# Kernel tuning notes

Measured on AMD Instinct MI355X. Metric: run time of the kernel, lower is better.

Reference implementation:

```python
import jax, jax.numpy as jnp
import numpy as np

HIDDEN = 1024
NUM_EXPERTS = 8
TOP_K = 2
B, S = 4, 2048


def setup_inputs() -> dict:
    key = jax.random.key(0)
    ks = jax.random.split(key, 7)
    s = 0.02
    return {
        "x": jax.random.normal(ks[0], (B, S, HIDDEN), dtype=jnp.float32),
        "gate_w": jax.random.normal(ks[1], (NUM_EXPERTS, HIDDEN), dtype=jnp.float32) * s,
        "gate_b": jnp.zeros((NUM_EXPERTS,), dtype=jnp.float32),
        "w1": jax.random.normal(ks[2], (NUM_EXPERTS, 4 * HIDDEN, HIDDEN), dtype=jnp.float32) * s,
        "b1": jnp.zeros((NUM_EXPERTS, 4 * HIDDEN), dtype=jnp.float32),
        "w2": jax.random.normal(ks[3], (NUM_EXPERTS, HIDDEN, 4 * HIDDEN), dtype=jnp.float32) * s,
        "b2": jnp.zeros((NUM_EXPERTS, HIDDEN), dtype=jnp.float32),
    }


def reference(x, gate_w, gate_b, w1, b1, w2, b2):
    bsz, seq_len, hidden = x.shape
    T = bsz * seq_len
    flat = x.reshape(T, hidden)  # [T, H]

    gate_logits = flat @ gate_w.T + gate_b  # [T, E]
    topk_vals, topk_idx = jax.lax.top_k(gate_logits, TOP_K)  # [T, K]
    topk_w = jax.nn.softmax(topk_vals, axis=-1)  # [T, K]

    # combine[t, e] = routing weight of expert e for token t (0 if not selected)
    combine = jnp.zeros((T, NUM_EXPERTS), dtype=flat.dtype)
    combine = combine.at[jnp.arange(T)[:, None], topk_idx].add(topk_w)

    out_flat = jnp.zeros_like(flat)
    for e in range(NUM_EXPERTS):  # small fixed expert count
        h = jax.nn.gelu(flat @ w1[e].T + b1[e], approximate=False)  # [T, 4H]
        y = h @ w2[e].T + b2[e]  # [T, H]
        out_flat = out_flat + y * combine[:, e:e + 1]

    out = out_flat.reshape(bsz, seq_len, hidden)
    probs = jax.nn.softmax(gate_logits, axis=-1).mean(axis=0)  # [E]
    l_aux = (probs * probs).sum() * NUM_EXPERTS
    return out, l_aux
```

## Files before the change

### kernel.cpp

```cpp
#include <hip/hip_runtime.h>
#include <cstdint>
#include <cstddef>

typedef unsigned short u16;
typedef short bf16x8 __attribute__((ext_vector_type(8)));
typedef float f32x4 __attribute__((ext_vector_type(4)));
typedef u16 u16x4 __attribute__((ext_vector_type(4)));

#define NTOK 8192
#define HID 1024
#define NEXP 8
#define FF 4096
#define MAXPAIR 18432

__device__ __forceinline__ u16 bf16_rne(float f) {
  unsigned u = __builtin_bit_cast(unsigned, f);
  return (u16)((u + 0x7FFFu + ((u >> 16) & 1u)) >> 16);
}

__device__ __forceinline__ float gelu_tanh(float v) {
  const float u = 0.7978845608028654f * (v + 0.044715f * v * v * v);
  const float e = __expf(2.0f * u);
  return v - v * __frcp_rn(e + 1.0f);
}

__device__ __forceinline__ void async16(const void* g, void* l) {
  __builtin_amdgcn_global_load_lds(
      (const __attribute__((address_space(1))) void*)g,
      (__attribute__((address_space(3))) void*)l, 16, 0, 0);
}

__global__ __launch_bounds__(256) void gate_kernel(
    const float* __restrict__ x, const float* __restrict__ gw,
    const float* __restrict__ gb, int* __restrict__ counts,
    float* __restrict__ probs_sum, int* __restrict__ topk_e,
    float* __restrict__ topk_w) {
  __shared__ float sgw[NEXP * HID];
  __shared__ float sProbs[NEXP];
  __shared__ int sCnt[NEXP];
  const int tid = threadIdx.x;
  for (int i = tid; i < NEXP * HID; i += 256) sgw[i] = gw[i];
  if (tid < NEXP) { sProbs[tid] = 0.f; sCnt[tid] = 0; }
  __syncthreads();
  const int lane = tid & 63, wave = tid >> 6;
  for (int it = 0; it < 4; ++it) {
    const int t = blockIdx.x * 16 + wave * 4 + it;
    const float* xr = x + (size_t)t * HID;
    float a[NEXP];
#pragma unroll
    for (int e = 0; e < NEXP; ++e) a[e] = 0.f;
    for (int j = 0; j < 16; ++j) {
      const int o = lane + 64 * j;
      const float v = xr[o];
#pragma unroll
      for (int e = 0; e < NEXP; ++e) a[e] += v * sgw[e * HID + o];
    }
#pragma unroll
    for (int off = 32; off > 0; off >>= 1)
#pragma unroll
      for (int e = 0; e < NEXP; ++e) a[e] += __shfl_xor(a[e], off);
    if (lane == 0) {
      float l[NEXP];
#pragma unroll
      for (int e = 0; e < NEXP; ++e) l[e] = a[e] + gb[e];
      int b0 = 0; float v0 = l[0];
#pragma unroll
      for (int e = 1; e < NEXP; ++e) if (l[e] > v0) { b0 = e; v0 = l[e]; }
      int b1i = (b0 == 0) ? 1 : 0; float v1 = l[b1i];
#pragma unroll
      for (int e = 0; e < NEXP; ++e) if (e != b0 && l[e] > v1) { b1i = e; v1 = l[e]; }
      const float e1 = __expf(v1 - v0);
      const float inv01 = 1.f / (1.f + e1);
      topk_e[2 * t] = b0; topk_e[2 * t + 1] = b1i;
      topk_w[2 * t] = inv01; topk_w[2 * t + 1] = e1 * inv01;
      atomicAdd(&sCnt[b0], 1); atomicAdd(&sCnt[b1i], 1);
      float s = 0.f, p[NEXP];
#pragma unroll
      for (int e = 0; e < NEXP; ++e) { p[e] = __expf(l[e] - v0); s += p[e]; }
      const float invs = 1.f / s;
#pragma unroll
      for (int e = 0; e < NEXP; ++e) atomicAdd(&sProbs[e], p[e] * invs);
    }
  }
  __syncthreads();
  if (tid < NEXP) {
    atomicAdd(&counts[tid], sCnt[tid]);
    atomicAdd(&probs_sum[tid], sProbs[tid]);
  }
}

__global__ void finalize_kernel(const int* __restrict__ counts,
                                int* __restrict__ cursors,
                                int* __restrict__ offsets,
                                const float* __restrict__ probs_sum,
                                float* __restrict__ laux) {
  if (threadIdx.x == 0) {
    int off = 0;
    for (int e = 0; e < NEXP; ++e) {
      offsets[e] = off;
      off += ((counts[e] + 255) / 256) * 256;
      cursors[e] = 0;
    }
    offsets[NEXP] = off;
    float s = 0.f;
    for (int e = 0; e < NEXP; ++e) {
      const float p = probs_sum[e] * (1.f / (float)NTOK);
      s += p * p;
    }
    *laux = (float)NEXP * s;
  }
}

__global__ __launch_bounds__(256) void scatter_kernel(
    const int* __restrict__ topk_e, const float* __restrict__ topk_w,
    const int* __restrict__ offsets, int* __restrict__ cursors,
    int* __restrict__ tok_of_pair, float* __restrict__ wt_of_pair,
    int* __restrict__ slot_of_tok) {
  __shared__ int lcnt[NEXP], lbase[NEXP];
  const int tid = threadIdx.x;
  if (tid < NEXP) lcnt[tid] = 0;
  __syncthreads();
  const int t = blockIdx.x * 256 + tid;
  const int e0 = topk_e[2 * t], e1 = topk_e[2 * t + 1];
  const int p0 = atomicAdd(&lcnt[e0], 1);
  const int p1 = atomicAdd(&lcnt[e1], 1);
  __syncthreads();
  if (tid < NEXP) lbase[tid] = atomicAdd(&cursors[tid], lcnt[tid]);
  __syncthreads();
  const int s0 = offsets[e0] + lbase[e0] + p0;
  const int s1 = offsets[e1] + lbase[e1] + p1;
  tok_of_pair[s0] = t; wt_of_pair[s0] = topk_w[2 * t];
  tok_of_pair[s1] = t; wt_of_pair[s1] = topk_w[2 * t + 1];
  slot_of_tok[2 * t] = s0; slot_of_tok[2 * t + 1] = s1;
}

__global__ __launch_bounds__(256) void stream_cvt_kernel(const float4* __restrict__ src,
                                                         u16x4* __restrict__ dst) {
  const int i = blockIdx.x * 256 + threadIdx.x;
  const float4 v = src[i];
  u16x4 o;
  o[0] = bf16_rne(v.x); o[1] = bf16_rne(v.y); o[2] = bf16_rne(v.z); o[3] = bf16_rne(v.w);
  dst[i] = o;
}

template <bool P1>
__global__ __launch_bounds__(512, 2) void moe_gemm(
    const u16* __restrict__ Aop,
    const u16* __restrict__ Bop,
    const float* __restrict__ b1,
    const int* __restrict__ tok_of_pair,
    const int* __restrict__ offsets,
    u16* __restrict__ hout,
    float* __restrict__ ypair) {
  constexpr int LDK  = P1 ? HID : FF;
  constexpr int NOUT = P1 ? FF : HID;
  constexpr int T    = LDK / 32;
  constexpr int NT   = NOUT / 256;
  __shared__ u16 As[4][8192];
  __shared__ u16 Bs[4][8192];

  const int cpx = (int)gridDim.x >> 3;
  const int orig = ((int)blockIdx.x & 7) * cpx + ((int)blockIdx.x >> 3);
  const int nt = orig % NT, mt = orig / NT;

  const int base = mt * 256;
  if (base >= offsets[NEXP]) return;
  int e = 0;
  while (e < NEXP - 1 && base >= offsets[e + 1]) ++e;
  const int tid = threadIdx.x;
  const int lane = tid & 63;
  const int wave = tid >> 6;
  const int wm = wave & 1, wn = wave >> 1;

  const int gl = (tid & 7) ^ ((tid >> 3) & 7);
  const int rS = ((tid >> 3) << 1) | (gl >> 2);
  const int cS = (gl & 3) * 8;
  const u16 *gA0, *gA1;
  if constexpr (P1) {
    gA0 = Aop + (size_t)tok_of_pair[base + rS] * LDK + cS;
    gA1 = Aop + (size_t)tok_of_pair[base + rS + 128] * LDK + cS;
  } else {
    gA0 = Aop + (size_t)(base + rS) * LDK + cS;
    gA1 = Aop + (size_t)(base + rS + 128) * LDK + cS;
  }
  const u16* wBb = Bop + (size_t)e * ((size_t)NOUT * LDK) + (size_t)(nt * 256) * LDK;
  const u16* gB0 = wBb + (size_t)rS * LDK + cS;
  const u16* gB1 = wBb + (size_t)(rS + 128) * LDK + cS;

#define STAGE_A(step) { u16* d_ = &As[(step) & 3][0]; const int k_ = (step) * 32; \
    async16(gA0 + k_, d_ + (size_t)tid * 8); async16(gA1 + k_, d_ + ((size_t)tid + 512) * 8); }
#define STAGE_B(step) { u16* d_ = &Bs[(step) & 3][0]; const int k_ = (step) * 32; \
    async16(gB0 + k_, d_ + (size_t)tid * 8); async16(gB1 + k_, d_ + ((size_t)tid + 512) * 8); }

  STAGE_A(0); STAGE_B(0); STAGE_A(1); STAGE_B(1); STAGE_A(2); STAGE_B(2);
  asm volatile("s_waitcnt vmcnt(8)" ::: "memory");
  __builtin_amdgcn_s_barrier();
  __builtin_amdgcn_sched_barrier(0);

  const int nl = lane & 15, q = lane >> 4;
  const int rdS = (((((nl & 1) << 2) | q) ^ (nl >> 1))) * 8;
  const int aB = (wm * 64 + (nl >> 1)) * 64 + rdS;
  const int bB = (wn * 32 + (nl >> 1)) * 64 + rdS;

  f32x4 acc[8][4];
#pragma unroll
  for (int i = 0; i < 8; ++i)
#pragma unroll
    for (int j = 0; j < 4; ++j) acc[i][j] = (f32x4){0.f, 0.f, 0.f, 0.f};

#pragma unroll 1
  for (int t = 0; t < T; ++t) {
    const u16* A = &As[t & 3][0];
    const u16* B = &Bs[t & 3][0];
    const bool pf = (t + 3 < T);
    bf16x8 af[4], bf[4];
#pragma unroll
    for (int i = 0; i < 4; ++i) af[i] = *(const bf16x8*)&A[aB + i * 512];
#pragma unroll
    for (int j = 0; j < 4; ++j) bf[j] = *(const bf16x8*)&B[bB + j * 512];
    if (pf) STAGE_A(t + 3);
    __builtin_amdgcn_s_barrier();
    __builtin_amdgcn_sched_barrier(0);
    __builtin_amdgcn_s_setprio(1);
#pragma unroll
    for (int i = 0; i < 4; ++i)
#pragma unroll
      for (int j = 0; j < 4; ++j)
        acc[i][j] = __builtin_amdgcn_mfma_f32_16x16x32_bf16(af[i], bf[j], acc[i][j], 0, 0, 0);
    __builtin_amdgcn_s_setprio(0);
    __builtin_amdgcn_s_barrier();
    __builtin_amdgcn_sched_barrier(0);
#pragma unroll
    for (int i = 0; i < 4; ++i) af[i] = *(const bf16x8*)&A[aB + 2048 + i * 512];
    if (pf) STAGE_B(t + 3);
    __builtin_amdgcn_s_barrier();
    __builtin_amdgcn_sched_barrier(0);
    __builtin_amdgcn_s_setprio(1);
#pragma unroll
    for (int i = 0; i < 4; ++i)
#pragma unroll
      for (int j = 0; j < 4; ++j)
        acc[4 + i][j] = __builtin_amdgcn_mfma_f32_16x16x32_bf16(af[i], bf[j], acc[4 + i][j], 0, 0, 0);
    __builtin_amdgcn_s_setprio(0);
    if (t + 4 <= T)      { asm volatile("s_waitcnt vmcnt(8)" ::: "memory"); }
    else if (t + 3 == T) { asm volatile("s_waitcnt vmcnt(4)" ::: "memory"); }
    else if (t + 2 == T) { asm volatile("s_waitcnt vmcnt(0)" ::: "memory"); }
    __builtin_amdgcn_s_barrier();
    __builtin_amdgcn_sched_barrier(0);
  }
#undef STAGE_A
#undef STAGE_B

  const int rowq = q * 4;
  if constexpr (P1) {
    const float* b1e = b1 + (size_t)e * FF;
#pragma unroll
    for (int j = 0; j < 4; ++j) {
      const int n = nt * 256 + wn * 64 + j * 16 + nl;
      const float bias = b1e[n];
#pragma unroll
      for (int i = 0; i < 8; ++i) {
        const int m = base + wm * 128 + i * 16 + rowq;
#pragma unroll
        for (int r = 0; r < 4; ++r)
          hout[(size_t)(m + r) * FF + n] = bf16_rne(gelu_tanh(acc[i][j][r] + bias));
      }
    }
  } else {
#pragma unroll
    for (int i = 0; i < 8; ++i) {
      const int m = base + wm * 128 + i * 16 + rowq;
#pragma unroll
      for (int r = 0; r < 4; ++r) {
        float* yrow = ypair + (size_t)(m + r) * HID + nt * 256 + wn * 64;
#pragma unroll
        for (int j = 0; j < 4; ++j) yrow[j * 16 + nl] = acc[i][j][r];
      }
    }
  }
}

__global__ __launch_bounds__(256) void combine_kernel(
    const float* __restrict__ ypair, const int* __restrict__ slot_of_tok,
    const int* __restrict__ topk_e, const float* __restrict__ topk_w,
    const float* __restrict__ b2, float* __restrict__ out) {
  const int t = blockIdx.x;
  const int tid = threadIdx.x;
  const int s0 = slot_of_tok[2 * t], s1 = slot_of_tok[2 * t + 1];
  const int e0 = topk_e[2 * t], e1 = topk_e[2 * t + 1];
  const float w0 = topk_w[2 * t], w1v = topk_w[2 * t + 1];
  const float4 y0 = ((const float4*)(ypair + (size_t)s0 * HID))[tid];
  const float4 y1 = ((const float4*)(ypair + (size_t)s1 * HID))[tid];
  const float4 c0 = ((const float4*)(b2 + (size_t)e0 * HID))[tid];
  const float4 c1 = ((const float4*)(b2 + (size_t)e1 * HID))[tid];
  float4 o;
  o.x = w0 * (y0.x + c0.x) + w1v * (y1.x + c1.x);
  o.y = w0 * (y0.y + c0.y) + w1v * (y1.y + c1.y);
  o.z = w0 * (y0.z + c0.z) + w1v * (y1.z + c1.z);
  o.w = w0 * (y0.w + c0.w) + w1v * (y1.w + c1.w);
  ((float4*)(out + (size_t)t * HID))[tid] = o;
}

extern "C" void kernel_launch(void* const* d_in, const int* in_sizes, int n_in,
                              void* d_out, int out_size, void* d_ws, size_t ws_size,
                              hipStream_t stream) {
  (void)in_sizes; (void)n_in; (void)ws_size;
  const float* x  = (const float*)d_in[0];
  const float* gw = (const float*)d_in[1];
  const float* gb = (const float*)d_in[2];
  const float* w1 = (const float*)d_in[3];
  const float* b1 = (const float*)d_in[4];
  const float* w2 = (const float*)d_in[5];
  const float* b2 = (const float*)d_in[6];
  float* out = (float*)d_out;

  char* ws = (char*)d_ws;
  int*   counts  = (int*)(ws + 0);
  int*   cursors = (int*)(ws + 32);
  float* probs   = (float*)(ws + 64);
  int*   offsets = (int*)(ws + 96);
  int*   tok     = (int*)(ws + 4096);
  float* wt      = (float*)(ws + 77824);
  int*   topk_e  = (int*)(ws + 151552);
  float* topk_w  = (float*)(ws + 217088);
  int*   slot    = (int*)(ws + 282624);
  u16*   xb    = (u16*)(ws + 1048576);
  u16*   w1b   = (u16*)(ws + 17825792);
  u16*   w2b   = (u16*)(ws + 84934656);
  u16*   hbuf  = (u16*)(ws + 152043520);
  float* ypair = (float*)(ws + 1048576);

  hipMemsetAsync(ws, 0, 348160, stream);

  gate_kernel<<<512, 256, 0, stream>>>(x, gw, gb, counts, probs, topk_e, topk_w);
  finalize_kernel<<<1, 64, 0, stream>>>(counts, cursors, offsets, probs,
                                        out + (out_size - 1));
  scatter_kernel<<<32, 256, 0, stream>>>(topk_e, topk_w, offsets, cursors, tok, wt, slot);
  stream_cvt_kernel<<<8192, 256, 0, stream>>>((const float4*)x, (u16x4*)xb);
  stream_cvt_kernel<<<32768, 256, 0, stream>>>((const float4*)w1, (u16x4*)w1b);
  stream_cvt_kernel<<<32768, 256, 0, stream>>>((const float4*)w2, (u16x4*)w2b);

  const int MT = MAXPAIR / 256;
  moe_gemm<true><<<(FF / 256) * MT, 512, 0, stream>>>(
      xb, w1b, b1, tok, offsets, hbuf, nullptr);
  moe_gemm<false><<<(HID / 256) * MT, 512, 0, stream>>>(
      hbuf, w2b, nullptr, tok, offsets, nullptr, ypair);
  combine_kernel<<<8192, 256, 0, stream>>>(ypair, slot, topk_e, topk_w, b2, out);
}
```

Baseline: 881.9 us.

## Collapse two-phase MFMA main loop into single phase with fewer barriers

```diff
diff --git a/kernel.cpp b/kernel.cpp
--- a/kernel.cpp
+++ b/kernel.cpp
@@ -212,36 +212,25 @@
   for (int t = 0; t < T; ++t) {
     const u16* A = &As[t & 3][0];
     const u16* B = &Bs[t & 3][0];
-    const bool pf = (t + 3 < T);
-    bf16x8 af[4], bf[4];
+    if (t + 3 < T) { STAGE_A(t + 3); STAGE_B(t + 3); }
+    bf16x8 af[4], ag[4], bf[4];
+#pragma unroll
+    for (int j = 0; j < 4; ++j) bf[j] = *(const bf16x8*)&B[bB + j * 512];
 #pragma unroll
     for (int i = 0; i < 4; ++i) af[i] = *(const bf16x8*)&A[aB + i * 512];
 #pragma unroll
-    for (int j = 0; j < 4; ++j) bf[j] = *(const bf16x8*)&B[bB + j * 512];
-    if (pf) STAGE_A(t + 3);
-    __builtin_amdgcn_s_barrier();
-    __builtin_amdgcn_sched_barrier(0);
-    __builtin_amdgcn_s_setprio(1);
+    for (int i = 0; i < 4; ++i) ag[i] = *(const bf16x8*)&A[aB + 2048 + i * 512];
 #pragma unroll
     for (int i = 0; i < 4; ++i)
 #pragma unroll
       for (int j = 0; j < 4; ++j)
         acc[i][j] = __builtin_amdgcn_mfma_f32_16x16x32_bf16(af[i], bf[j], acc[i][j], 0, 0, 0);
-    __builtin_amdgcn_s_setprio(0);
-    __builtin_amdgcn_s_barrier();
+#pragma unroll
+    for (int i = 0; i < 4; ++i)
+#pragma unroll
+      for (int j = 0; j < 4; ++j)
+        acc[4 + i][j] = __builtin_amdgcn_mfma_f32_16x16x32_bf16(ag[i], bf[j], acc[4 + i][j], 0, 0, 0);
     __builtin_amdgcn_sched_barrier(0);
-#pragma unroll
-    for (int i = 0; i < 4; ++i) af[i] = *(const bf16x8*)&A[aB + 2048 + i * 512];
-    if (pf) STAGE_B(t + 3);
-    __builtin_amdgcn_s_barrier();
-    __builtin_amdgcn_sched_barrier(0);
-    __builtin_amdgcn_s_setprio(1);
-#pragma unroll
-    for (int i = 0; i < 4; ++i)
-#pragma unroll
-      for (int j = 0; j < 4; ++j)
-        acc[4 + i][j] = __builtin_amdgcn_mfma_f32_16x16x32_bf16(af[i], bf[j], acc[4 + i][j], 0, 0, 0);
-    __builtin_amdgcn_s_setprio(0);
     if (t + 4 <= T)      { asm volatile("s_waitcnt vmcnt(8)" ::: "memory"); }
     else if (t + 3 == T) { asm volatile("s_waitcnt vmcnt(4)" ::: "memory"); }
     else if (t + 2 == T) { asm volatile("s_waitcnt vmcnt(0)" ::: "memory"); }
@@ -253,26 +242,28 @@
 
   const int rowq = q * 4;
   if constexpr (P1) {
-    const float* b1e = b1 + (size_t)e * FF;
-#pragma unroll
-    for (int j = 0; j < 4; ++j) {
-      const int n = nt * 256 + wn * 64 + j * 16 + nl;
-      const float bias = b1e[n];
-#pragma unroll
-      for (int i = 0; i < 8; ++i) {
-        const int m = base + wm * 128 + i * 16 + rowq;
-#pragma unroll
-        for (int r = 0; r < 4; ++r)
-          hout[(size_t)(m + r) * FF + n] = bf16_rne(gelu_tanh(acc[i][j][r] + bias));
+    const float* b1e = b1 + (size_t)e * FF + nt * 256 + wn * 64;
+    float bias[4];
+#pragma unroll
+    for (int j = 0; j < 4; ++j) bias[j] = b1e[j * 16 + nl];
+#pragma unroll
+    for (int i = 0; i < 8; ++i) {
+#pragma unroll
+      for (int r = 0; r < 4; ++r) {
+        const int m = base + wm * 128 + i * 16 + rowq + r;
+        u16* hrow = hout + (size_t)m * FF + nt * 256 + wn * 64;
+#pragma unroll
+        for (int j = 0; j < 4; ++j)
+          hrow[j * 16 + nl] = bf16_rne(gelu_tanh(acc[i][j][r] + bias[j]));
       }
     }
   } else {
 #pragma unroll
     for (int i = 0; i < 8; ++i) {
-      const int m = base + wm * 128 + i * 16 + rowq;
 #pragma unroll
       for (int r = 0; r < 4; ++r) {
-        float* yrow = ypair + (size_t)(m + r) * HID + nt * 256 + wn * 64;
+        const int m = base + wm * 128 + i * 16 + rowq + r;
+        float* yrow = ypair + (size_t)m * HID + nt * 256 + wn * 64;
 #pragma unroll
         for (int j = 0; j < 4; ++j) yrow[j * 16 + nl] = acc[i][j][r];
       }
```

Result: slower. 991.1 us (+12.4%).
